# Performance work log

Measured on AMD Instinct MI355X. Metric: run time of the kernel, lower is better.

Reference implementation:

```python
import jax, jax.numpy as jnp
import numpy as np

B = 2
D = 256
NH = 8
DH = D // NH
LV = 4
NP_ = 4
NL = 6
DFF = 1024
SHAPES = [(112, 112), (56, 56), (28, 28), (14, 14)]
S = sum(h * w for h, w in SHAPES)


def setup_inputs() -> dict:
    key = jax.random.key(0)
    ks = iter(jax.random.split(key, 64))
    d = {}
    for i, (h, w) in enumerate(SHAPES):
        d[f"src{i}"] = jax.random.normal(next(ks), (B, D, h, w), jnp.float32)
        d[f"pos{i}"] = jax.random.normal(next(ks), (B, D, h, w), jnp.float32)

    def W(*shape, scale=0.02):
        return jax.random.normal(next(ks), shape, jnp.float32) * scale

    d["level_embed"] = W(LV, D, scale=1.0)
    d["off_w"] = W(NL, D, NH * LV * NP_ * 2)
    d["off_b"] = W(NL, NH * LV * NP_ * 2, scale=0.5)
    d["aw_w"] = W(NL, D, NH * LV * NP_)
    d["aw_b"] = jnp.zeros((NL, NH * LV * NP_), jnp.float32)
    d["val_w"] = W(NL, D, D)
    d["val_b"] = jnp.zeros((NL, D), jnp.float32)
    d["out_w"] = W(NL, D, D)
    d["out_b"] = jnp.zeros((NL, D), jnp.float32)
    d["ln1_s"] = jnp.ones((NL, D), jnp.float32)
    d["ln1_b"] = jnp.zeros((NL, D), jnp.float32)
    d["ff1_w"] = W(NL, D, DFF)
    d["ff1_b"] = jnp.zeros((NL, DFF), jnp.float32)
    d["ff2_w"] = W(NL, DFF, D)
    d["ff2_b"] = jnp.zeros((NL, D), jnp.float32)
    d["ln2_s"] = jnp.ones((NL, D), jnp.float32)
    d["ln2_b"] = jnp.zeros((NL, D), jnp.float32)
    return d


def _ln(x, s, b):
    m = jnp.mean(x, -1, keepdims=True)
    v = jnp.mean((x - m) ** 2, -1, keepdims=True)
    return (x - m) / jnp.sqrt(v + 1e-5) * s + b


def _bilinear(v, loc, Hl, Wl):
    # v: [N, DH, Hl, Wl]; loc: [N, Q, P, 2] in [0,1] (grid_sample align_corners=False, zero padding)
    N, Dh = v.shape[0], v.shape[1]
    Q, P = loc.shape[1], loc.shape[2]
    x = loc[..., 0] * Wl - 0.5
    y = loc[..., 1] * Hl - 0.5
    x0f = jnp.floor(x)
    y0f = jnp.floor(y)
    lx = x - x0f
    ly = y - y0f
    x0 = x0f.astype(jnp.int32)
    y0 = y0f.astype(jnp.int32)
    vf = v.reshape(N, Dh, Hl * Wl)

    def g(xi, yi):
        valid = (xi >= 0) & (xi < Wl) & (yi >= 0) & (yi < Hl)
        idx = (jnp.clip(yi, 0, Hl - 1) * Wl + jnp.clip(xi, 0, Wl - 1)).reshape(N, Q * P)
        out = jnp.take_along_axis(vf, idx[:, None, :], axis=2).reshape(N, Dh, Q, P)
        return out * valid[:, None].astype(v.dtype)

    w00 = ((1 - lx) * (1 - ly))[:, None]
    w10 = (lx * (1 - ly))[:, None]
    w01 = ((1 - lx) * ly)[:, None]
    w11 = (lx * ly)[:, None]
    return g(x0, y0) * w00 + g(x0 + 1, y0) * w10 + g(x0, y0 + 1) * w01 + g(x0 + 1, y0 + 1) * w11


def _ms_deform_attn(value, loc, attn):
    # value [B,S,NH,DH], loc [B,S,NH,LV,P,2], attn [B,S,NH,LV,P]
    out = jnp.zeros((B * NH, DH, S), value.dtype)
    s0 = 0
    for l, (Hl, Wl) in enumerate(SHAPES):
        vl = value[:, s0:s0 + Hl * Wl].reshape(B, Hl, Wl, NH, DH)
        vl = vl.transpose(0, 3, 4, 1, 2).reshape(B * NH, DH, Hl, Wl)
        ll = loc[:, :, :, l].transpose(0, 2, 1, 3, 4).reshape(B * NH, S, NP_, 2)
        al = attn[:, :, :, l].transpose(0, 2, 1, 3).reshape(B * NH, S, NP_)[:, None]
        out = out + (_bilinear(vl, ll, Hl, Wl) * al).sum(-1)
        s0 += Hl * Wl
    return out.reshape(B, NH * DH, S).transpose(0, 2, 1)


def _forward(srcs, poss, level_embed, off_w, off_b, aw_w, aw_b, val_w, val_b,
             out_w, out_b, ln1_s, ln1_b, ff1_w, ff1_b, ff2_w, ff2_b, ln2_s, ln2_b):
    src = jnp.concatenate([s.reshape(B, D, -1).transpose(0, 2, 1) for s in srcs], 1)
    pos = jnp.concatenate(
        [p.reshape(B, D, -1).transpose(0, 2, 1) + level_embed[i][None, None] for i, p in enumerate(poss)], 1)
    # reference points: padding masks are all-False => valid_ratios == 1
    refs = []
    for (Hl, Wl) in SHAPES:
        gy, gx = jnp.meshgrid((jnp.arange(Hl) + 0.5) / Hl, (jnp.arange(Wl) + 0.5) / Wl, indexing="ij")
        refs.append(jnp.stack([gx.ravel(), gy.ravel()], -1))
    ref = jnp.concatenate(refs, 0)  # [S, 2]
    normalizer = jnp.array([[w, h] for (h, w) in SHAPES], jnp.float32)  # [LV, 2] = (W, H)
    x = src
    for i in range(NL):
        q = x + pos
        off = (q @ off_w[i] + off_b[i]).reshape(B, S, NH, LV, NP_, 2)
        aw = jax.nn.softmax((q @ aw_w[i] + aw_b[i]).reshape(B, S, NH, LV * NP_), -1)
        aw = aw.reshape(B, S, NH, LV, NP_)
        val = (x @ val_w[i] + val_b[i]).reshape(B, S, NH, DH)
        loc = ref[None, :, None, None, None, :] + off / normalizer[None, None, None, :, None, :]
        attn_out = _ms_deform_attn(val, loc, aw) @ out_w[i] + out_b[i]
        x = _ln(x + attn_out, ln1_s[i], ln1_b[i])
        ff = jax.nn.relu(x @ ff1_w[i] + ff1_b[i]) @ ff2_w[i] + ff2_b[i]
        x = _ln(x + ff, ln2_s[i], ln2_b[i])
    return x


def reference(src0, src1, src2, src3, pos0, pos1, pos2, pos3, level_embed,
              off_w, off_b, aw_w, aw_b, val_w, val_b, out_w, out_b,
              ln1_s, ln1_b, ff1_w, ff1_b, ff2_w, ff2_b, ln2_s, ln2_b):
    memory = _forward([src0, src1, src2, src3], [pos0, pos1, pos2, pos3], level_embed,
                      off_w, off_b, aw_w, aw_b, val_w, val_b, out_w, out_b,
                      ln1_s, ln1_b, ff1_w, ff1_b, ff2_w, ff2_b, ln2_s, ln2_b)
    spatial_shapes = jnp.array(SHAPES, jnp.int32)
    level_start_index = jnp.concatenate(
        [jnp.zeros((1,), jnp.int32), jnp.cumsum(spatial_shapes.prod(1))[:-1].astype(jnp.int32)])
    return memory, spatial_shapes, level_start_index
```

## Files before the change

kernel.cpp:

```cpp
#include <hip/hip_runtime.h>


constexpr int kB  = 2;
constexpr int kD  = 256;
constexpr int kNH = 8;
constexpr int kLV = 4;
constexpr int kNP = 4;
constexpr int kNL = 6;
constexpr int kDFF = 1024;
constexpr int kS  = 16660;
constexpr int kM  = kB * kS;
constexpr int kMp = 33408;
constexpr int kMT = kMp / 128;
constexpr int kMT64 = kMp / 64;
constexpr int kMT32 = kMp / 32;

typedef short bf16x8 __attribute__((ext_vector_type(8)));
typedef float f32x4  __attribute__((ext_vector_type(4)));

__device__ __forceinline__ unsigned short f2bf(float x) {
  union { float f; unsigned int u; } v; v.f = x;
  unsigned int r = v.u + 0x7FFFu + ((v.u >> 16) & 1u);
  return (unsigned short)(r >> 16);
}
__device__ __forceinline__ float bf2f(unsigned short u) {
  union { unsigned int u; float f; } v; v.u = ((unsigned int)u) << 16;
  return v.f;
}

#define GLOAD_LDS16(gp, lp)                                                    \
  __builtin_amdgcn_global_load_lds(                                            \
      (const __attribute__((address_space(1))) void*)(gp),                     \
      (__attribute__((address_space(3))) void*)(lp), 16, 0, 0)

__global__ __launch_bounds__(256) void build_xpos_k(
    const float* __restrict__ src, const float* __restrict__ pos,
    const float* __restrict__ lemb, float* __restrict__ xout,
    float* __restrict__ posout, unsigned short* __restrict__ xbf,
    unsigned short* __restrict__ qbf, int HW, int s0, int lvl)
{
  __shared__ float ts[32][33];
  __shared__ float tp[32][33];
  const int b  = blockIdx.z;
  const int p0 = blockIdx.x * 32, d0 = blockIdx.y * 32;
  const int tx = threadIdx.x, ty = threadIdx.y;
  for (int dd = ty; dd < 32; dd += 8) {
    int p = p0 + tx;
    if (p < HW) {
      size_t idx = ((size_t)b * kD + (d0 + dd)) * (size_t)HW + p;
      ts[dd][tx] = src[idx];
      tp[dd][tx] = pos[idx];
    }
  }
  __syncthreads();
  for (int pp = ty; pp < 32; pp += 8) {
    int p = p0 + pp, d = d0 + tx;
    if (p < HW) {
      size_t o = ((size_t)b * kS + (s0 + p)) * (size_t)kD + d;
      float x = ts[tx][pp];
      float pv = tp[tx][pp] + lemb[lvl * kD + d];
      xout[o] = x;
      posout[o] = pv;
      xbf[o] = f2bf(x);
      qbf[o] = f2bf(x + pv);
    }
  }
}

__global__ __launch_bounds__(256) void wconv_k(
    const float* __restrict__ W, unsigned short* __restrict__ Wt,
    int K, int N, int rowoff, int rowstotal)
{
  __shared__ float t[32][33];
  const int l = blockIdx.z;
  const int n0 = blockIdx.x * 32, k0 = blockIdx.y * 32;
  const int tx = threadIdx.x & 31, ty = threadIdx.x >> 5;
  const float* Wl = W + (size_t)l * K * N;
  unsigned short* Wtl = Wt + (size_t)l * rowstotal * K;
  for (int kk = ty; kk < 32; kk += 8)
    t[kk][tx] = Wl[(size_t)(k0 + kk) * N + n0 + tx];
  __syncthreads();
  for (int nn = ty; nn < 32; nn += 8)
    Wtl[(size_t)(rowoff + n0 + nn) * K + k0 + tx] = f2bf(t[tx][nn]);
}

__global__ __launch_bounds__(256) void biaspack_k(
    const float* __restrict__ ob, const float* __restrict__ ab,
    float* __restrict__ qb)
{
  int i = blockIdx.x * 256 + threadIdx.x;
  if (i >= kNL * 384) return;
  int l = i / 384, c = i - l * 384;
  qb[i] = (c < 256) ? ob[l * 256 + c] : ab[l * 128 + (c - 256)];
}

template<int RELU, int OUTBF>
__global__ __launch_bounds__(256) void hgemm_k(
    const unsigned short* __restrict__ A, const unsigned short* __restrict__ Bt,
    const float* __restrict__ bias, void* __restrict__ Cout, int N, int K)
{
  __shared__ unsigned short As[128 * 32];
  __shared__ unsigned short Bs[128 * 32];
  const int tid = threadIdx.x;
  const int bm = blockIdx.y * 128;
  const int bn = blockIdx.x * 128;
  const int lane = tid & 63;
  const int wave = tid >> 6;
  const int wr = (wave >> 1) * 64, wc = (wave & 1) * 64;
  const int l15 = lane & 15, l4 = lane >> 4;

  f32x4 acc[4][4] = {};

  const int c0 = tid, c1 = 256 + tid;
  const int r0 = c0 >> 2, kk0 = (c0 & 3) << 3;
  const int r1 = c1 >> 2, kk1 = (c1 & 3) << 3;
  const unsigned short* A0 = A + (size_t)(bm + r0) * K + kk0;
  const unsigned short* A1 = A + (size_t)(bm + r1) * K + kk1;
  const unsigned short* B0 = Bt + (size_t)(bn + r0) * K + kk0;
  const unsigned short* B1 = Bt + (size_t)(bn + r1) * K + kk1;

  for (int k0 = 0; k0 < K; k0 += 32) {
    GLOAD_LDS16(A0 + k0, (char*)As + c0 * 16);
    GLOAD_LDS16(A1 + k0, (char*)As + c1 * 16);
    GLOAD_LDS16(B0 + k0, (char*)Bs + c0 * 16);
    GLOAD_LDS16(B1 + k0, (char*)Bs + c1 * 16);
    __syncthreads();
    bf16x8 af[4], bfr[4];
#pragma unroll
    for (int m = 0; m < 4; ++m)
      af[m] = *(const bf16x8*)&As[(wr + m * 16 + l15) * 32 + l4 * 8];
#pragma unroll
    for (int n = 0; n < 4; ++n)
      bfr[n] = *(const bf16x8*)&Bs[(wc + n * 16 + l15) * 32 + l4 * 8];
#pragma unroll
    for (int m = 0; m < 4; ++m)
#pragma unroll
      for (int n = 0; n < 4; ++n)
        acc[m][n] = __builtin_amdgcn_mfma_f32_16x16x32_bf16(
            af[m], bfr[n], acc[m][n], 0, 0, 0);
    __syncthreads();
  }

#pragma unroll
  for (int n = 0; n < 4; ++n) {
    const int col = bn + wc + n * 16 + l15;
    const float bv = bias[col];
#pragma unroll
    for (int m = 0; m < 4; ++m) {
#pragma unroll
      for (int j = 0; j < 4; ++j) {
        const int row = bm + wr + m * 16 + l4 * 4 + j;
        float v = acc[m][n][j] + bv;
        if (RELU) v = fmaxf(v, 0.f);
        if (OUTBF)
          ((unsigned short*)Cout)[(size_t)row * N + col] = f2bf(v);
        else
          ((float*)Cout)[(size_t)row * N + col] = v;
      }
    }
  }
}

template<int OUTBF>
__global__ __launch_bounds__(256) void hgemm64_k(
    const unsigned short* __restrict__ A, const unsigned short* __restrict__ Bt,
    const float* __restrict__ bias, void* __restrict__ Cout, int N, int K)
{
  __shared__ unsigned short As[2][64 * 32];
  __shared__ unsigned short Bs[2][128 * 32];
  const int tid = threadIdx.x;
  const int bm = blockIdx.y * 64;
  const int bn = blockIdx.x * 128;
  const int lane = tid & 63;
  const int wave = tid >> 6;
  const int wr = (wave >> 1) * 32, wc = (wave & 1) * 64;
  const int l15 = lane & 15, l4 = lane >> 4;

  f32x4 acc[2][4] = {};

  const unsigned short* A0 = A + (size_t)(bm + (tid >> 2)) * K + ((tid & 3) << 3);
  const int cb1 = 256 + tid;
  const unsigned short* B0 = Bt + (size_t)(bn + (tid >> 2)) * K + ((tid & 3) << 3);
  const unsigned short* B1 = Bt + (size_t)(bn + (cb1 >> 2)) * K + ((cb1 & 3) << 3);

#define STAGE64(buf, k0)                                                       \
  do {                                                                         \
    GLOAD_LDS16(A0 + (k0), (char*)As[buf] + tid * 16);                         \
    GLOAD_LDS16(B0 + (k0), (char*)Bs[buf] + tid * 16);                         \
    GLOAD_LDS16(B1 + (k0), (char*)Bs[buf] + cb1 * 16);                         \
  } while (0)

  STAGE64(0, 0);
  __syncthreads();
  int cur = 0;
  for (int k0 = 0; k0 < K; k0 += 32) {
    if (k0 + 32 < K) STAGE64(cur ^ 1, k0 + 32);
    bf16x8 af[2], bfr[4];
#pragma unroll
    for (int m = 0; m < 2; ++m)
      af[m] = *(const bf16x8*)&As[cur][(wr + m * 16 + l15) * 32 + l4 * 8];
#pragma unroll
    for (int n = 0; n < 4; ++n)
      bfr[n] = *(const bf16x8*)&Bs[cur][(wc + n * 16 + l15) * 32 + l4 * 8];
#pragma unroll
    for (int m = 0; m < 2; ++m)
#pragma unroll
      for (int n = 0; n < 4; ++n)
        acc[m][n] = __builtin_amdgcn_mfma_f32_16x16x32_bf16(
            af[m], bfr[n], acc[m][n], 0, 0, 0);
    __syncthreads();
    cur ^= 1;
  }
#undef STAGE64

#pragma unroll
  for (int n = 0; n < 4; ++n) {
    const int col = bn + wc + n * 16 + l15;
    const float bv = bias[col];
#pragma unroll
    for (int m = 0; m < 2; ++m) {
#pragma unroll
      for (int j = 0; j < 4; ++j) {
        const int row = bm + wr + m * 16 + l4 * 4 + j;
        float v = acc[m][n][j] + bv;
        if (OUTBF)
          ((unsigned short*)Cout)[(size_t)row * N + col] = f2bf(v);
        else
          ((float*)Cout)[(size_t)row * N + col] = v;
      }
    }
  }
}

template<int WQ, int OUTDST>
__global__ __launch_bounds__(256) void hgemmln_k(
    const unsigned short* __restrict__ A, const unsigned short* __restrict__ Bt,
    const float* __restrict__ bias, const float* __restrict__ Rsd,
    const float* __restrict__ g, const float* __restrict__ beta,
    const float* __restrict__ posb, float* __restrict__ yout,
    unsigned short* __restrict__ xbf, unsigned short* __restrict__ qbf, int K)
{
  __shared__ unsigned short As[2][32 * 32];
  __shared__ unsigned short Bs[2][256 * 32];
  __shared__ float ssum[32][5];
  __shared__ float ssq[32][5];
  const int tid = threadIdx.x;
  const int bm = blockIdx.x * 32;
  const int lane = tid & 63;
  const int wave = tid >> 6;
  const int wc = wave * 64;
  const int l15 = lane & 15, l4 = lane >> 4;

  f32x4 acc[2][4] = {};

  const unsigned short* Aq = A + (size_t)(bm + (tid >> 2)) * K + ((tid & 3) << 3);
  const unsigned short* Bq0 = Bt + (size_t)(0 * 64 + (tid >> 2)) * K + ((tid & 3) << 3);
  const unsigned short* Bq1 = Bt + (size_t)(1 * 64 + (tid >> 2)) * K + ((tid & 3) << 3);
  const unsigned short* Bq2 = Bt + (size_t)(2 * 64 + (tid >> 2)) * K + ((tid & 3) << 3);
  const unsigned short* Bq3 = Bt + (size_t)(3 * 64 + (tid >> 2)) * K + ((tid & 3) << 3);

#define STAGE_LN(buf, k0)                                                      \
  do {                                                                         \
    if (tid < 128) GLOAD_LDS16(Aq + (k0), (char*)As[buf] + tid * 16);          \
    GLOAD_LDS16(Bq0 + (k0), (char*)Bs[buf] + (0 * 256 + tid) * 16);            \
    GLOAD_LDS16(Bq1 + (k0), (char*)Bs[buf] + (1 * 256 + tid) * 16);            \
    GLOAD_LDS16(Bq2 + (k0), (char*)Bs[buf] + (2 * 256 + tid) * 16);            \
    GLOAD_LDS16(Bq3 + (k0), (char*)Bs[buf] + (3 * 256 + tid) * 16);            \
  } while (0)

  STAGE_LN(0, 0);
  __syncthreads();
  int cur = 0;
  for (int k0 = 0; k0 < K; k0 += 32) {
    if (k0 + 32 < K) STAGE_LN(cur ^ 1, k0 + 32);
    bf16x8 af[2], bfr[4];
#pragma unroll
    for (int m = 0; m < 2; ++m)
      af[m] = *(const bf16x8*)&As[cur][(m * 16 + l15) * 32 + l4 * 8];
#pragma unroll
    for (int n = 0; n < 4; ++n)
      bfr[n] = *(const bf16x8*)&Bs[cur][(wc + n * 16 + l15) * 32 + l4 * 8];
#pragma unroll
    for (int m = 0; m < 2; ++m)
#pragma unroll
      for (int n = 0; n < 4; ++n)
        acc[m][n] = __builtin_amdgcn_mfma_f32_16x16x32_bf16(
            af[m], bfr[n], acc[m][n], 0, 0, 0);
    __syncthreads();
    cur ^= 1;
  }
#undef STAGE_LN

  float bv[4], gv[4], btv[4];
#pragma unroll
  for (int n = 0; n < 4; ++n) {
    const int col = wc + n * 16 + l15;
    bv[n] = bias[col];
    gv[n] = g[col];
    btv[n] = beta[col];
  }
#pragma unroll
  for (int m = 0; m < 2; ++m) {
#pragma unroll
    for (int j = 0; j < 4; ++j) {
      const int row = bm + m * 16 + l4 * 4 + j;
#pragma unroll
      for (int n = 0; n < 4; ++n)
        acc[m][n][j] += bv[n] + Rsd[(size_t)row * kD + wc + n * 16 + l15];
    }
  }
#pragma unroll
  for (int m = 0; m < 2; ++m) {
#pragma unroll
    for (int j = 0; j < 4; ++j) {
      float s = acc[m][0][j] + acc[m][1][j] + acc[m][2][j] + acc[m][3][j];
      float q = acc[m][0][j] * acc[m][0][j] + acc[m][1][j] * acc[m][1][j] +
                acc[m][2][j] * acc[m][2][j] + acc[m][3][j] * acc[m][3][j];
#pragma unroll
      for (int d2 = 1; d2 < 16; d2 <<= 1) {
        s += __shfl_xor(s, d2, 64);
        q += __shfl_xor(q, d2, 64);
      }
      if (l15 == 0) {
        const int r = m * 16 + l4 * 4 + j;
        ssum[r][wave] = s;
        ssq[r][wave] = q;
      }
    }
  }
  __syncthreads();
#pragma unroll
  for (int m = 0; m < 2; ++m) {
#pragma unroll
    for (int j = 0; j < 4; ++j) {
      const int r = m * 16 + l4 * 4 + j;
      const int row = bm + r;
      const float mean = (ssum[r][0] + ssum[r][1] + ssum[r][2] + ssum[r][3]) *
                         (1.0f / kD);
      const float var = (ssq[r][0] + ssq[r][1] + ssq[r][2] + ssq[r][3]) *
                        (1.0f / kD) - mean * mean;
      const float rstd = rsqrtf(var + 1e-5f);
      if (row < kM) {
#pragma unroll
        for (int n = 0; n < 4; ++n) {
          const int col = wc + n * 16 + l15;
          const float y = (acc[m][n][j] - mean) * rstd * gv[n] + btv[n];
          const size_t o = (size_t)row * kD + col;
          if (OUTDST) {
            yout[o] = y;
          } else {
            yout[o] = y;
            xbf[o] = f2bf(y);
            if (WQ) qbf[o] = f2bf(y + posb[o]);
          }
        }
      }
    }
  }
}

__global__ __launch_bounds__(256) void msdeform_k(
    const unsigned short* __restrict__ val, const float* __restrict__ qout,
    unsigned short* __restrict__ outbf)
{
  __shared__ int   sIdx[4][4][128];
  __shared__ float sW[4][4][128];
  const int bs0 = blockIdx.x * 4;
  const int tid = threadIdx.x;

#pragma unroll
  for (int it = 0; it < 2; ++it) {
    const int item = tid + it * 256;
    const int q = item >> 7;
    const int t = item & 127;
    const int bs = bs0 + q;
    const int b = bs / kS, s = bs - b * kS;
    const int l = (t & 15) >> 2;

    const float logit = qout[(size_t)bs * 384 + 256 + t];
    float mx = logit;
#pragma unroll
    for (int d2 = 1; d2 < 16; d2 <<= 1) mx = fmaxf(mx, __shfl_xor(mx, d2, 64));
    float e = __expf(logit - mx);
    float sm = e;
#pragma unroll
    for (int d2 = 1; d2 < 16; d2 <<= 1) sm += __shfl_xor(sm, d2, 64);
    const float a = e / sm;

    int ls, sideq;
    if (s < 12544)      { ls = s;         sideq = 112; }
    else if (s < 15680) { ls = s - 12544; sideq = 56;  }
    else if (s < 16464) { ls = s - 15680; sideq = 28;  }
    else                { ls = s - 16464; sideq = 14;  }
    const float rx = ((ls % sideq) + 0.5f) / (float)sideq;
    const float ry = ((ls / sideq) + 0.5f) / (float)sideq;

    const int side  = 112 >> l;
    const int start = (l >= 1 ? 12544 : 0) + (l >= 2 ? 3136 : 0) + (l >= 3 ? 784 : 0);
    const float ox = qout[(size_t)bs * 384 + t * 2 + 0];
    const float oy = qout[(size_t)bs * 384 + t * 2 + 1];
    const float xx = rx * side + ox - 0.5f;
    const float yy = ry * side + oy - 0.5f;
    const float xf = floorf(xx), yf = floorf(yy);
    const float lx = xx - xf, ly = yy - yf;
    const int x0 = (int)xf, y0 = (int)yf;
    const float w00 = (1.f - lx) * (1.f - ly) * a, w10 = lx * (1.f - ly) * a;
    const float w01 = (1.f - lx) * ly * a,         w11 = lx * ly * a;
    const bool xv0 = (unsigned)x0 < (unsigned)side, xv1 = (unsigned)(x0 + 1) < (unsigned)side;
    const bool yv0 = (unsigned)y0 < (unsigned)side, yv1 = (unsigned)(y0 + 1) < (unsigned)side;
    const int cx0 = min(max(x0, 0), side - 1), cx1 = min(max(x0 + 1, 0), side - 1);
    const int cy0 = min(max(y0, 0), side - 1), cy1 = min(max(y0 + 1, 0), side - 1);
    const int rowbase = b * kS + start;
    const int t2 = (t & 15) * 8 + (t >> 4);
    sIdx[0][q][t2] = rowbase + cy0 * side + cx0;
    sIdx[1][q][t2] = rowbase + cy0 * side + cx1;
    sIdx[2][q][t2] = rowbase + cy1 * side + cx0;
    sIdx[3][q][t2] = rowbase + cy1 * side + cx1;
    sW[0][q][t2] = (xv0 && yv0) ? w00 : 0.f;
    sW[1][q][t2] = (xv1 && yv0) ? w10 : 0.f;
    sW[2][q][t2] = (xv0 && yv1) ? w01 : 0.f;
    sW[3][q][t2] = (xv1 && yv1) ? w11 : 0.f;
  }
  __syncthreads();

  const int q  = tid >> 6;
  const int h  = (tid >> 3) & 7;
  const int l8 = tid & 7;
  const unsigned short* vb = val + h * 32 + l8 * 4;

  float a0 = 0.f, a1 = 0.f, a2 = 0.f, a3 = 0.f;
#pragma unroll
  for (int sp = 0; sp < 16; ++sp) {
    const int t2 = sp * 8 + h;
#pragma unroll
    for (int c = 0; c < 4; ++c) {
      const int r = sIdx[c][q][t2];
      const float w = sW[c][q][t2];
      const ushort4 v4 = *(const ushort4*)(vb + (size_t)r * 256);
      a0 = fmaf(w, bf2f(v4.x), a0);
      a1 = fmaf(w, bf2f(v4.y), a1);
      a2 = fmaf(w, bf2f(v4.z), a2);
      a3 = fmaf(w, bf2f(v4.w), a3);
    }
  }
  ushort4 o;
  o.x = f2bf(a0); o.y = f2bf(a1); o.z = f2bf(a2); o.w = f2bf(a3);
  *(ushort4*)(outbf + (size_t)(bs0 + q) * 256 + h * 32 + l8 * 4) = o;
}

__global__ void tail_k(float* __restrict__ out)
{
  if (threadIdx.x == 0) {
    const size_t n = (size_t)kM * kD;
    out[n + 0] = 112.f; out[n + 1] = 112.f;
    out[n + 2] = 56.f;  out[n + 3] = 56.f;
    out[n + 4] = 28.f;  out[n + 5] = 28.f;
    out[n + 6] = 14.f;  out[n + 7] = 14.f;
    out[n + 8] = 0.f;   out[n + 9] = 12544.f;
    out[n + 10] = 15680.f; out[n + 11] = 16464.f;
  }
}

extern "C" void kernel_launch(void* const* d_in, const int* in_sizes, int n_in,
                              void* d_out, int out_size, void* d_ws, size_t ws_size,
                              hipStream_t stream)
{
  const float* src[4] = {(const float*)d_in[0], (const float*)d_in[2],
                         (const float*)d_in[4], (const float*)d_in[6]};
  const float* pos[4] = {(const float*)d_in[1], (const float*)d_in[3],
                         (const float*)d_in[5], (const float*)d_in[7]};
  const float* lemb  = (const float*)d_in[8];
  const float* off_w = (const float*)d_in[9];
  const float* off_b = (const float*)d_in[10];
  const float* aw_w  = (const float*)d_in[11];
  const float* aw_b  = (const float*)d_in[12];
  const float* val_w = (const float*)d_in[13];
  const float* val_b = (const float*)d_in[14];
  const float* out_w = (const float*)d_in[15];
  const float* out_b = (const float*)d_in[16];
  const float* ln1_s = (const float*)d_in[17];
  const float* ln1_b = (const float*)d_in[18];
  const float* ff1_w = (const float*)d_in[19];
  const float* ff1_b = (const float*)d_in[20];
  const float* ff2_w = (const float*)d_in[21];
  const float* ff2_b = (const float*)d_in[22];
  const float* ln2_s = (const float*)d_in[23];
  const float* ln2_b = (const float*)d_in[24];

  const size_t SZ = (size_t)kMp * kD;
  float* ws   = (float*)d_ws;
  float* posb = (float*)d_out;
  float* xb   = ws;
  float* R    = ws + SZ;
  float* qout = R;
  unsigned short* valbf = (unsigned short*)(R + SZ + SZ / 2);
  unsigned short* attbf = (unsigned short*)(R + 2 * SZ);
  unsigned short* ffbf  = (unsigned short*)R;
  unsigned short* qbf   = (unsigned short*)(ws + 3 * SZ + SZ / 2);
  unsigned short* xbf   = qbf + SZ;
  unsigned short* wts   = (unsigned short*)(ws + 4 * SZ + SZ / 2);
  unsigned short* qwT  = wts;
  unsigned short* valT = qwT + kNL * 384 * 256;
  unsigned short* outT = valT + kNL * 256 * 256;
  unsigned short* ff1T = outT + kNL * 256 * 256;
  unsigned short* ff2T = ff1T + kNL * 1024 * 256;
  float* qbias = (float*)(ff2T + kNL * 256 * 1024);

  wconv_k<<<dim3(256 / 32, 256 / 32, kNL), 256, 0, stream>>>(off_w, qwT, 256, 256, 0, 384);
  wconv_k<<<dim3(128 / 32, 256 / 32, kNL), 256, 0, stream>>>(aw_w,  qwT, 256, 128, 256, 384);
  wconv_k<<<dim3(256 / 32, 256 / 32, kNL), 256, 0, stream>>>(val_w, valT, 256, 256, 0, 256);
  wconv_k<<<dim3(256 / 32, 256 / 32, kNL), 256, 0, stream>>>(out_w, outT, 256, 256, 0, 256);
  wconv_k<<<dim3(1024 / 32, 256 / 32, kNL), 256, 0, stream>>>(ff1_w, ff1T, 256, 1024, 0, 1024);
  wconv_k<<<dim3(256 / 32, 1024 / 32, kNL), 256, 0, stream>>>(ff2_w, ff2T, 1024, 256, 0, 256);
  biaspack_k<<<(kNL * 384 + 255) / 256, 256, 0, stream>>>(off_b, aw_b, qbias);

  const int sides[4]  = {112, 56, 28, 14};
  const int starts[4] = {0, 12544, 15680, 16464};
  for (int l = 0; l < 4; ++l) {
    int HW = sides[l] * sides[l];
    dim3 g((HW + 31) / 32, kD / 32, kB);
    build_xpos_k<<<g, dim3(32, 8), 0, stream>>>(src[l], pos[l], lemb, xb, posb,
                                                xbf, qbf, HW, starts[l], l);
  }

  const dim3 blk(256);
  for (int i = 0; i < kNL; ++i) {
    hgemm64_k<0><<<dim3(3, kMT64), blk, 0, stream>>>(
        qbf, qwT + (size_t)i * 384 * 256, qbias + i * 384, qout, 384, 256);
    hgemm64_k<1><<<dim3(2, kMT64), blk, 0, stream>>>(
        xbf, valT + (size_t)i * 256 * 256, val_b + i * 256, valbf, 256, 256);
    msdeform_k<<<kM / 4, blk, 0, stream>>>(valbf, qout, attbf);
    hgemmln_k<0, 0><<<kMT32, blk, 0, stream>>>(
        attbf, outT + (size_t)i * 256 * 256, out_b + i * 256, xb,
        ln1_s + i * kD, ln1_b + i * kD, nullptr, xb, xbf, nullptr, 256);
    hgemm_k<1, 1><<<dim3(8, kMT), blk, 0, stream>>>(
        xbf, ff1T + (size_t)i * 1024 * 256, ff1_b + i * 1024, ffbf, 1024, 256);
    if (i < kNL - 1) {
      hgemmln_k<1, 0><<<kMT32, blk, 0, stream>>>(
          ffbf, ff2T + (size_t)i * 256 * 1024, ff2_b + i * 256, xb,
          ln2_s + i * kD, ln2_b + i * kD, posb, xb, xbf, qbf, 1024);
    } else {
      hgemmln_k<0, 1><<<kMT32, blk, 0, stream>>>(
          ffbf, ff2T + (size_t)i * 256 * 1024, ff2_b + i * 256, xb,
          ln2_s + i * kD, ln2_b + i * kD, nullptr, (float*)d_out, nullptr,
          nullptr, 1024);
    }
  }

  tail_k<<<1, 64, 0, stream>>>((float*)d_out);
}
```

Before: 1.510 ms.

## Fuse query/value GEMMs, double-buffer FF1 GEMM, widen deformable-attention gathers

Merges the offset/attention-weight projection and the value projection into one launch that picks its operands from the block x index. The FF1 GEMM now uses 64-row double-buffered tiles instead of single-buffered 128-row tiles. The deformable sampling kernel issues 16-byte gathers with precomputed byte offsets, splits the four corners across lane pairs and combines them with a shuffle. The aims are fewer launches, more blocks with overlapped loads, and fewer, wider gather instructions, at the cost of less reuse per tile and extra shuffle work.

Result: slower. 1.566 ms (+3.7%).

```diff
diff --git a/kernel.cpp b/kernel.cpp
--- a/kernel.cpp
+++ b/kernel.cpp
@@ -11,7 +11,6 @@
 constexpr int kS  = 16660;
 constexpr int kM  = kB * kS;
 constexpr int kMp = 33408;
-constexpr int kMT = kMp / 128;
 constexpr int kMT64 = kMp / 64;
 constexpr int kMT32 = kMp / 32;
 
@@ -25,6 +24,14 @@
 }
 __device__ __forceinline__ float bf2f(unsigned short u) {
   union { unsigned int u; float f; } v; v.u = ((unsigned int)u) << 16;
+  return v.f;
+}
+__device__ __forceinline__ float bflo(unsigned int u) {
+  union { unsigned int u; float f; } v; v.u = u << 16;
+  return v.f;
+}
+__device__ __forceinline__ float bfhi(unsigned int u) {
+  union { unsigned int u; float f; } v; v.u = u & 0xFFFF0000u;
   return v.f;
 }
 
@@ -95,58 +102,63 @@
 }
 
 template<int RELU, int OUTBF>
-__global__ __launch_bounds__(256) void hgemm_k(
+__global__ __launch_bounds__(256) void hgemm64_k(
     const unsigned short* __restrict__ A, const unsigned short* __restrict__ Bt,
     const float* __restrict__ bias, void* __restrict__ Cout, int N, int K)
 {
-  __shared__ unsigned short As[128 * 32];
-  __shared__ unsigned short Bs[128 * 32];
+  __shared__ unsigned short As[2][64 * 32];
+  __shared__ unsigned short Bs[2][128 * 32];
   const int tid = threadIdx.x;
-  const int bm = blockIdx.y * 128;
+  const int bm = blockIdx.y * 64;
   const int bn = blockIdx.x * 128;
   const int lane = tid & 63;
   const int wave = tid >> 6;
-  const int wr = (wave >> 1) * 64, wc = (wave & 1) * 64;
+  const int wr = (wave >> 1) * 32, wc = (wave & 1) * 64;
   const int l15 = lane & 15, l4 = lane >> 4;
 
-  f32x4 acc[4][4] = {};
-
-  const int c0 = tid, c1 = 256 + tid;
-  const int r0 = c0 >> 2, kk0 = (c0 & 3) << 3;
-  const int r1 = c1 >> 2, kk1 = (c1 & 3) << 3;
-  const unsigned short* A0 = A + (size_t)(bm + r0) * K + kk0;
-  const unsigned short* A1 = A + (size_t)(bm + r1) * K + kk1;
-  const unsigned short* B0 = Bt + (size_t)(bn + r0) * K + kk0;
-  const unsigned short* B1 = Bt + (size_t)(bn + r1) * K + kk1;
-
+  f32x4 acc[2][4] = {};
+
+  const unsigned short* A0 = A + (size_t)(bm + (tid >> 2)) * K + ((tid & 3) << 3);
+  const int cb1 = 256 + tid;
+  const unsigned short* B0 = Bt + (size_t)(bn + (tid >> 2)) * K + ((tid & 3) << 3);
+  const unsigned short* B1 = Bt + (size_t)(bn + (cb1 >> 2)) * K + ((cb1 & 3) << 3);
+
+#define STAGE64(buf, k0)                                                       \
+  do {                                                                         \
+    GLOAD_LDS16(A0 + (k0), (char*)As[buf] + tid * 16);                         \
+    GLOAD_LDS16(B0 + (k0), (char*)Bs[buf] + tid * 16);                         \
+    GLOAD_LDS16(B1 + (k0), (char*)Bs[buf] + cb1 * 16);                         \
+  } while (0)
+
+  STAGE64(0, 0);
+  __syncthreads();
+  int cur = 0;
   for (int k0 = 0; k0 < K; k0 += 32) {
-    GLOAD_LDS16(A0 + k0, (char*)As + c0 * 16);
-    GLOAD_LDS16(A1 + k0, (char*)As + c1 * 16);
-    GLOAD_LDS16(B0 + k0, (char*)Bs + c0 * 16);
-    GLOAD_LDS16(B1 + k0, (char*)Bs + c1 * 16);
-    __syncthreads();
-    bf16x8 af[4], bfr[4];
-#pragma unroll
-    for (int m = 0; m < 4; ++m)
-      af[m] = *(const bf16x8*)&As[(wr + m * 16 + l15) * 32 + l4 * 8];
+    if (k0 + 32 < K) STAGE64(cur ^ 1, k0 + 32);
+    bf16x8 af[2], bfr[4];
+#pragma unroll
+    for (int m = 0; m < 2; ++m)
+      af[m] = *(const bf16x8*)&As[cur][(wr + m * 16 + l15) * 32 + l4 * 8];
 #pragma unroll
     for (int n = 0; n < 4; ++n)
-      bfr[n] = *(const bf16x8*)&Bs[(wc + n * 16 + l15) * 32 + l4 * 8];
-#pragma unroll
-    for (int m = 0; m < 4; ++m)
+      bfr[n] = *(const bf16x8*)&Bs[cur][(wc + n * 16 + l15) * 32 + l4 * 8];
+#pragma unroll
+    for (int m = 0; m < 2; ++m)
 #pragma unroll
       for (int n = 0; n < 4; ++n)
         acc[m][n] = __builtin_amdgcn_mfma_f32_16x16x32_bf16(
             af[m], bfr[n], acc[m][n], 0, 0, 0);
     __syncthreads();
-  }
+    cur ^= 1;
+  }
+#undef STAGE64
 
 #pragma unroll
   for (int n = 0; n < 4; ++n) {
     const int col = bn + wc + n * 16 + l15;
     const float bv = bias[col];
 #pragma unroll
-    for (int m = 0; m < 4; ++m) {
+    for (int m = 0; m < 2; ++m) {
 #pragma unroll
       for (int j = 0; j < 4; ++j) {
         const int row = bm + wr + m * 16 + l4 * 4 + j;
@@ -161,16 +173,24 @@
   }
 }
 
-template<int OUTBF>
-__global__ __launch_bounds__(256) void hgemm64_k(
-    const unsigned short* __restrict__ A, const unsigned short* __restrict__ Bt,
-    const float* __restrict__ bias, void* __restrict__ Cout, int N, int K)
-{
+__global__ __launch_bounds__(256) void qvgemm_k(
+    const unsigned short* __restrict__ Aq, const unsigned short* __restrict__ Ax,
+    const unsigned short* __restrict__ Bq, const unsigned short* __restrict__ Bv,
+    const float* __restrict__ biasq, const float* __restrict__ biasv,
+    float* __restrict__ Cq, unsigned short* __restrict__ Cv)
+{
+  constexpr int K = 256;
   __shared__ unsigned short As[2][64 * 32];
   __shared__ unsigned short Bs[2][128 * 32];
   const int tid = threadIdx.x;
+  const int bx = blockIdx.x;
+  const bool isv = bx >= 3;
+  const int bn = (isv ? bx - 3 : bx) * 128;
   const int bm = blockIdx.y * 64;
-  const int bn = blockIdx.x * 128;
+  const unsigned short* A  = isv ? Ax : Aq;
+  const unsigned short* Bt = isv ? Bv : Bq;
+  const float* bias = isv ? biasv : biasq;
+  const int N = isv ? 256 : 384;
   const int lane = tid & 63;
   const int wave = tid >> 6;
   const int wr = (wave >> 1) * 32, wc = (wave & 1) * 64;
@@ -183,18 +203,19 @@
   const unsigned short* B0 = Bt + (size_t)(bn + (tid >> 2)) * K + ((tid & 3) << 3);
   const unsigned short* B1 = Bt + (size_t)(bn + (cb1 >> 2)) * K + ((cb1 & 3) << 3);
 
-#define STAGE64(buf, k0)                                                       \
+#define STAGEQV(buf, k0)                                                       \
   do {                                                                         \
     GLOAD_LDS16(A0 + (k0), (char*)As[buf] + tid * 16);                         \
     GLOAD_LDS16(B0 + (k0), (char*)Bs[buf] + tid * 16);                         \
     GLOAD_LDS16(B1 + (k0), (char*)Bs[buf] + cb1 * 16);                         \
   } while (0)
 
-  STAGE64(0, 0);
+  STAGEQV(0, 0);
   __syncthreads();
   int cur = 0;
+#pragma unroll
   for (int k0 = 0; k0 < K; k0 += 32) {
-    if (k0 + 32 < K) STAGE64(cur ^ 1, k0 + 32);
+    if (k0 + 32 < K) STAGEQV(cur ^ 1, k0 + 32);
     bf16x8 af[2], bfr[4];
 #pragma unroll
     for (int m = 0; m < 2; ++m)
@@ -211,7 +232,7 @@
     __syncthreads();
     cur ^= 1;
   }
-#undef STAGE64
+#undef STAGEQV
 
 #pragma unroll
   for (int n = 0; n < 4; ++n) {
@@ -223,10 +244,10 @@
       for (int j = 0; j < 4; ++j) {
         const int row = bm + wr + m * 16 + l4 * 4 + j;
         float v = acc[m][n][j] + bv;
-        if (OUTBF)
-          ((unsigned short*)Cout)[(size_t)row * N + col] = f2bf(v);
+        if (isv)
+          Cv[(size_t)row * 256 + col] = f2bf(v);
         else
-          ((float*)Cout)[(size_t)row * N + col] = v;
+          Cq[(size_t)row * 384 + col] = v;
       }
     }
   }
@@ -412,10 +433,10 @@
     const int cy0 = min(max(y0, 0), side - 1), cy1 = min(max(y0 + 1, 0), side - 1);
     const int rowbase = b * kS + start;
     const int t2 = (t & 15) * 8 + (t >> 4);
-    sIdx[0][q][t2] = rowbase + cy0 * side + cx0;
-    sIdx[1][q][t2] = rowbase + cy0 * side + cx1;
-    sIdx[2][q][t2] = rowbase + cy1 * side + cx0;
-    sIdx[3][q][t2] = rowbase + cy1 * side + cx1;
+    sIdx[0][q][t2] = (rowbase + cy0 * side + cx0) * 512;
+    sIdx[1][q][t2] = (rowbase + cy0 * side + cx1) * 512;
+    sIdx[2][q][t2] = (rowbase + cy1 * side + cx0) * 512;
+    sIdx[3][q][t2] = (rowbase + cy1 * side + cx1) * 512;
     sW[0][q][t2] = (xv0 && yv0) ? w00 : 0.f;
     sW[1][q][t2] = (xv1 && yv0) ? w10 : 0.f;
     sW[2][q][t2] = (xv0 && yv1) ? w01 : 0.f;
@@ -423,29 +444,42 @@
   }
   __syncthreads();
 
-  const int q  = tid >> 6;
-  const int h  = (tid >> 3) & 7;
-  const int l8 = tid & 7;
-  const unsigned short* vb = val + h * 32 + l8 * 4;
+  const int q    = tid >> 6;
+  const int lane = tid & 63;
+  const int h    = lane >> 3;
+  const int l4   = (lane >> 1) & 3;
+  const int cp   = lane & 1;
+  const char* vbase = (const char*)val + h * 64 + l4 * 16;
 
   float a0 = 0.f, a1 = 0.f, a2 = 0.f, a3 = 0.f;
+  float a4 = 0.f, a5 = 0.f, a6 = 0.f, a7 = 0.f;
 #pragma unroll
   for (int sp = 0; sp < 16; ++sp) {
     const int t2 = sp * 8 + h;
 #pragma unroll
-    for (int c = 0; c < 4; ++c) {
-      const int r = sIdx[c][q][t2];
+    for (int j = 0; j < 2; ++j) {
+      const int c = 2 * cp + j;
+      const int off = sIdx[c][q][t2];
       const float w = sW[c][q][t2];
-      const ushort4 v4 = *(const ushort4*)(vb + (size_t)r * 256);
-      a0 = fmaf(w, bf2f(v4.x), a0);
-      a1 = fmaf(w, bf2f(v4.y), a1);
-      a2 = fmaf(w, bf2f(v4.z), a2);
-      a3 = fmaf(w, bf2f(v4.w), a3);
-    }
-  }
-  ushort4 o;
-  o.x = f2bf(a0); o.y = f2bf(a1); o.z = f2bf(a2); o.w = f2bf(a3);
-  *(ushort4*)(outbf + (size_t)(bs0 + q) * 256 + h * 32 + l8 * 4) = o;
+      const uint4 v = *(const uint4*)(vbase + off);
+      a0 = fmaf(w, bflo(v.x), a0); a1 = fmaf(w, bfhi(v.x), a1);
+      a2 = fmaf(w, bflo(v.y), a2); a3 = fmaf(w, bfhi(v.y), a3);
+      a4 = fmaf(w, bflo(v.z), a4); a5 = fmaf(w, bfhi(v.z), a5);
+      a6 = fmaf(w, bflo(v.w), a6); a7 = fmaf(w, bfhi(v.w), a7);
+    }
+  }
+  a0 += __shfl_xor(a0, 1, 64); a1 += __shfl_xor(a1, 1, 64);
+  a2 += __shfl_xor(a2, 1, 64); a3 += __shfl_xor(a3, 1, 64);
+  a4 += __shfl_xor(a4, 1, 64); a5 += __shfl_xor(a5, 1, 64);
+  a6 += __shfl_xor(a6, 1, 64); a7 += __shfl_xor(a7, 1, 64);
+  if (cp == 0) {
+    bf16x8 o;
+    o[0] = (short)f2bf(a0); o[1] = (short)f2bf(a1);
+    o[2] = (short)f2bf(a2); o[3] = (short)f2bf(a3);
+    o[4] = (short)f2bf(a4); o[5] = (short)f2bf(a5);
+    o[6] = (short)f2bf(a6); o[7] = (short)f2bf(a7);
+    *(bf16x8*)(outbf + (size_t)(bs0 + q) * 256 + h * 32 + l4 * 8) = o;
+  }
 }
 
 __global__ void tail_k(float* __restrict__ out)
@@ -525,15 +559,14 @@
 
   const dim3 blk(256);
   for (int i = 0; i < kNL; ++i) {
-    hgemm64_k<0><<<dim3(3, kMT64), blk, 0, stream>>>(
-        qbf, qwT + (size_t)i * 384 * 256, qbias + i * 384, qout, 384, 256);
-    hgemm64_k<1><<<dim3(2, kMT64), blk, 0, stream>>>(
-        xbf, valT + (size_t)i * 256 * 256, val_b + i * 256, valbf, 256, 256);
+    qvgemm_k<<<dim3(5, kMT64), blk, 0, stream>>>(
+        qbf, xbf, qwT + (size_t)i * 384 * 256, valT + (size_t)i * 256 * 256,
+        qbias + i * 384, val_b + i * 256, qout, valbf);
     msdeform_k<<<kM / 4, blk, 0, stream>>>(valbf, qout, attbf);
     hgemmln_k<0, 0><<<kMT32, blk, 0, stream>>>(
         attbf, outT + (size_t)i * 256 * 256, out_b + i * 256, xb,
         ln1_s + i * kD, ln1_b + i * kD, nullptr, xb, xbf, nullptr, 256);
-    hgemm_k<1, 1><<<dim3(8, kMT), blk, 0, stream>>>(
+    hgemm64_k<1, 1><<<dim3(8, kMT64), blk, 0, stream>>>(
         xbf, ff1T + (size_t)i * 1024 * 256, ff1_b + i * 1024, ffbf, 1024, 256);
     if (i < kNL - 1) {
       hgemmln_k<1, 0><<<kMT32, blk, 0, stream>>>(
```
